# Kernel tuning notes

Measured on AMD Instinct MI355X. Metric: run time of the kernel, lower is better.

Reference implementation:

```python
import jax, jax.numpy as jnp
import numpy as np

B, S, D, H, HS = 4, 2048, 1024, 16, 64
DFF = 4 * D
EPS = 1e-5


def setup_inputs() -> dict:
    key = jax.random.key(0)
    ks = jax.random.split(key, 16)
    std = 0.02
    return {
        "x": jax.random.normal(ks[0], (B, S, D), jnp.float32),
        "Wq": jax.random.normal(ks[1], (H, D, HS), jnp.float32) * std,
        "bq": jnp.zeros((H, HS), jnp.float32),
        "Wk": jax.random.normal(ks[2], (H, D, HS), jnp.float32) * std,
        "bk": jnp.zeros((H, HS), jnp.float32),
        "Wv": jax.random.normal(ks[3], (H, D, HS), jnp.float32) * std,
        "bv": jnp.zeros((H, HS), jnp.float32),
        "Wp": jax.random.normal(ks[4], (D, D), jnp.float32) * std,
        "bp": jnp.zeros((D,), jnp.float32),
        "ln1_w": jnp.ones((D,), jnp.float32),
        "ln1_b": jnp.zeros((D,), jnp.float32),
        "ln2_w": jnp.ones((D,), jnp.float32),
        "ln2_b": jnp.zeros((D,), jnp.float32),
        "W1": jax.random.normal(ks[5], (D, DFF), jnp.float32) * std,
        "b1": jnp.zeros((DFF,), jnp.float32),
        "W2": jax.random.normal(ks[6], (DFF, D), jnp.float32) * std,
        "b2": jnp.zeros((D,), jnp.float32),
    }


def _layernorm(x, w, b):
    mu = jnp.mean(x, axis=-1, keepdims=True)
    var = jnp.mean(jnp.square(x - mu), axis=-1, keepdims=True)
    return (x - mu) * jax.lax.rsqrt(var + EPS) * w + b


def _block(x, Wq, bq, Wk, bk, Wv, bv, Wp, bp, ln1_w, ln1_b, ln2_w, ln2_b, W1, b1, W2, b2):
    seq = x.shape[1]
    xn = _layernorm(x, ln1_w, ln1_b)
    # batched per-head projections: [B,H,S,HS]
    q = jnp.einsum('bsd,hdk->bhsk', xn, Wq) + bq[:, None, :]
    k = jnp.einsum('bsd,hdk->bhsk', xn, Wk) + bk[:, None, :]
    v = jnp.einsum('bsd,hdk->bhsk', xn, Wv) + bv[:, None, :]
    scores = jnp.einsum('bhsk,bhtk->bhst', q, k)
    mask = jnp.tril(jnp.ones((seq, seq), bool))
    # original: masked_fill(-inf) then divide by sqrt(head_size) -> equivalent
    scores = jnp.where(mask, scores / jnp.sqrt(jnp.float32(HS)), -jnp.inf)
    attn = jax.nn.softmax(scores, axis=-1)
    out = jnp.einsum('bhst,bhtk->bhsk', attn, v)
    out = out.transpose(0, 2, 1, 3).reshape(x.shape[0], seq, H * HS)
    att = out @ Wp + bp
    x = x + att
    xn2 = _layernorm(x, ln2_w, ln2_b)
    h = jax.nn.gelu(xn2 @ W1 + b1, approximate=False)  # torch nn.GELU default = exact
    ffn = h @ W2 + b2
    return x + ffn


def reference(x, Wq, bq, Wk, bk, Wv, bv, Wp, bp, ln1_w, ln1_b, ln2_w, ln2_b, W1, b1, W2, b2):
    out = _block(x, Wq, bq, Wk, bk, Wv, bv, Wp, bp, ln1_w, ln1_b, ln2_w, ln2_b, W1, b1, W2, b2)
    return out
```

## Files before the change

### kernel.cpp

```cpp
#include <hip/hip_runtime.h>
#include <hip/hip_bf16.h>

#define D_MODEL 1024
#define SEQ 2048
#define NH 16
#define HSZ 64
#define DFF_ 4096

typedef __attribute__((ext_vector_type(8))) short short8;
typedef __attribute__((ext_vector_type(4))) short short4v;
typedef __attribute__((ext_vector_type(4))) float f32x4;

static __device__ __forceinline__ short f2bf(float f) {
  unsigned u = __builtin_bit_cast(unsigned, f);
  u = u + 0x7fffu + ((u >> 16) & 1u);
  return (short)(u >> 16);
}

static __device__ __forceinline__ unsigned packbf2(float a, float b) {
  return (unsigned)(unsigned short)f2bf(a) | ((unsigned)(unsigned short)f2bf(b) << 16);
}

static __device__ __forceinline__ f32x4 mfma16(short8 a, short8 b, f32x4 c) {
  return __builtin_amdgcn_mfma_f32_16x16x32_bf16(a, b, c, 0, 0, 0);
}

static __device__ __forceinline__ void gld16(const short* g, short* l) {
  __builtin_amdgcn_global_load_lds((const __attribute__((address_space(1))) void*)g,
                                   (__attribute__((address_space(3))) void*)l, 16, 0, 0);
}

#define SM_SCALE 0.18033688011112042f
#define VMW(n) asm volatile("s_waitcnt vmcnt(" #n ")" ::: "memory")

__global__ void transpose_qkv_kernel(const float* __restrict__ Wq, const float* __restrict__ Wk,
                                     const float* __restrict__ Wv, short* __restrict__ dst) {
  __shared__ float tile[32][33];
  const int z = blockIdx.z;
  const int which = z >> 4, hh = z & 15;
  const float* src = (which == 0 ? Wq : which == 1 ? Wk : Wv) + (long)hh * (D_MODEL * HSZ);
  const int c0 = blockIdx.x * 32, r0 = blockIdx.y * 32;
  const int tx = threadIdx.x, ty = threadIdx.y;
#pragma unroll
  for (int i = 0; i < 4; ++i)
    tile[ty + 8 * i][tx] = src[(long)(r0 + ty + 8 * i) * HSZ + c0 + tx];
  __syncthreads();
#pragma unroll
  for (int i = 0; i < 4; ++i)
    dst[((long)which * 1024 + hh * 64 + c0 + ty + 8 * i) * D_MODEL + r0 + tx] =
        f2bf(tile[tx][ty + 8 * i]);
}

__global__ void transpose_all_kernel(const float* __restrict__ Wp, short* __restrict__ WpT,
                                     const float* __restrict__ W1, short* __restrict__ W1T,
                                     const float* __restrict__ W2, short* __restrict__ W2T) {
  __shared__ float tile[32][33];
  int id = blockIdx.x;
  const float* src;
  short* dst;
  int R, C, bx, by;
  if (id < 1024) {
    src = Wp; dst = WpT; R = 1024; C = 1024; bx = id & 31; by = id >> 5;
  } else if (id < 5120) {
    id -= 1024;
    src = W1; dst = W1T; R = 1024; C = 4096; bx = id & 127; by = id >> 7;
  } else {
    id -= 5120;
    src = W2; dst = W2T; R = 4096; C = 1024; bx = id & 31; by = id >> 5;
  }
  const int c0 = bx * 32, r0 = by * 32;
  const int tx = threadIdx.x, ty = threadIdx.y;
#pragma unroll
  for (int i = 0; i < 4; ++i)
    tile[ty + 8 * i][tx] = src[(long)(r0 + ty + 8 * i) * C + c0 + tx];
  __syncthreads();
#pragma unroll
  for (int i = 0; i < 4; ++i)
    dst[(long)(c0 + ty + 8 * i) * R + r0 + tx] = f2bf(tile[tx][ty + 8 * i]);
}

__global__ void v_transpose_kernel(const short* __restrict__ vb, short* __restrict__ vt) {
  __shared__ short tile[64 * 72];
  const int bh = blockIdx.y;
  const int t0 = blockIdx.x * 64;
  const long base = (long)bh * SEQ * HSZ;
  const int tid = threadIdx.x;
  const int r = tid >> 3, c = (tid & 7) * 8;
#pragma unroll
  for (int it = 0; it < 2; ++it) {
    const int rr = r + it * 32;
    *(short8*)&tile[rr * 72 + c] = *(const short8*)(vb + base + (long)(t0 + rr) * HSZ + c);
  }
  __syncthreads();
#pragma unroll
  for (int it = 0; it < 2; ++it) {
    const int rr = r + it * 32;
    short8 o;
#pragma unroll
    for (int u = 0; u < 8; ++u) o[u] = tile[(c + u) * 72 + rr];
    *(short8*)(vt + base + (long)rr * SEQ + t0 + c) = o;
  }
}

__global__ void ln_kernel(const float* __restrict__ x, const float* __restrict__ w,
                          const float* __restrict__ b, short* __restrict__ out) {
  const int row = blockIdx.x;
  const float* xr = x + (size_t)row * D_MODEL;
  const int t = threadIdx.x;
  float4 v = *(const float4*)(xr + t * 4);
  float s = v.x + v.y + v.z + v.w;
  float s2 = v.x * v.x + v.y * v.y + v.z * v.z + v.w * v.w;
#pragma unroll
  for (int o = 1; o < 64; o <<= 1) {
    s += __shfl_xor(s, o, 64);
    s2 += __shfl_xor(s2, o, 64);
  }
  __shared__ float ps[8];
  const int lane = t & 63, wid = t >> 6;
  if (lane == 0) { ps[wid] = s; ps[wid + 4] = s2; }
  __syncthreads();
  s = ps[0] + ps[1] + ps[2] + ps[3];
  s2 = ps[4] + ps[5] + ps[6] + ps[7];
  const float mu = s * (1.0f / D_MODEL);
  const float var = s2 * (1.0f / D_MODEL) - mu * mu;
  const float rs = rsqrtf(var + 1e-5f);
  float4 wv = *(const float4*)(w + t * 4);
  float4 bv = *(const float4*)(b + t * 4);
  short4v o4;
  o4[0] = f2bf((v.x - mu) * rs * wv.x + bv.x);
  o4[1] = f2bf((v.y - mu) * rs * wv.y + bv.y);
  o4[2] = f2bf((v.z - mu) * rs * wv.z + bv.z);
  o4[3] = f2bf((v.w - mu) * rs * wv.w + bv.w);
  *(short4v*)(out + (size_t)row * D_MODEL + t * 4) = o4;
}

template <int MODE, int BM>
__global__ __launch_bounds__(512, 2) void gemm_kernel(
    const short* __restrict__ A, const short* __restrict__ Bt, const int K,
    const float* __restrict__ c0, const float* __restrict__ c1,
    const float* __restrict__ c2, const float* __restrict__ res,
    void* __restrict__ o0, void* __restrict__ o1, void* __restrict__ o2) {
  constexpr int NPH = BM / 64;
  constexpr int NA = BM / 64;
  constexpr int NTOT = NA + 4;
  constexpr int PER = NTOT / NPH;
  constexpr int HM = BM / 2;
  __shared__ short As[2][BM * 64];
  __shared__ short Bs[2][256 * 64];
  const long r0 = (long)blockIdx.y * BM;
  const long n0 = (long)blockIdx.x * 256;
  const int tid = threadIdx.x;
  const int lane = tid & 63, wid = tid >> 6;
  const int wm = wid >> 2, wn = wid & 3;
  const int l16 = lane & 15, lg = lane >> 4;

  long offA[NA], offB[4];
#pragma unroll
  for (int i = 0; i < NA; ++i) {
    const int c = tid + i * 512;
    const int lam = c >> 3, s = c & 7;
    const int cch = lam >> 6, rho = lam & 63;
    const int g = cch * 32 + (rho & 31) + ((rho >> 5) ? HM : 0);
    offA[i] = (long)(r0 + g) * K + ((s ^ (lam & 7)) << 3);
  }
#pragma unroll
  for (int i = 0; i < 4; ++i) {
    const int c = tid + i * 512;
    const int row = c >> 3, s = c & 7;
    offB[i] = (long)(n0 + row) * K + ((s ^ (row & 7)) << 3);
  }

  f32x4 acc[2 * NPH][4];
#pragma unroll
  for (int m = 0; m < 2 * NPH; ++m)
#pragma unroll
    for (int n = 0; n < 4; ++n) {
      f32x4 z = {0.f, 0.f, 0.f, 0.f};
      acc[m][n] = z;
    }

  const int x7 = l16 & 7;
  const int sw0 = (lg ^ x7) * 8, sw1 = ((4 + lg) ^ x7) * 8;

#define STG(j, kt, buf)                                                      \
  {                                                                          \
    if ((j) < 4)                                                             \
      gld16(Bt + offB[(j)] + (kt), &Bs[buf][(tid + (j)*512) * 8]);           \
    else                                                                     \
      gld16(A + offA[(j)-4] + (kt), &As[buf][(tid + ((j)-4) * 512) * 8]);    \
  }

#define GPHASE(P, ENDSTMT)                                                   \
  {                                                                          \
    short8 af[2][2];                                                         \
    _Pragma("unroll") for (int mm = 0; mm < 2; ++mm) {                       \
      const int lam = (P)*64 + wm * 32 + mm * 16 + l16;                      \
      af[mm][0] = *(const short8*)&Ap[lam * 64 + sw0];                       \
      af[mm][1] = *(const short8*)&Ap[lam * 64 + sw1];                       \
    }                                                                        \
    if ((P) == 0) {                                                          \
      _Pragma("unroll") for (int n = 0; n < 4; ++n) {                        \
        const int r = (wn * 64 + n * 16 + l16) * 64;                         \
        bf[n][0] = *(const short8*)&Bp[r + sw0];                             \
        bf[n][1] = *(const short8*)&Bp[r + sw1];                             \
      }                                                                      \
    }                                                                        \
    if (st) {                                                                \
      _Pragma("unroll") for (int j = (P)*PER; j < ((P) + 1) * PER; ++j)      \
          STG(j, ktn, nb);                                                   \
    }                                                                        \
    asm volatile("s_waitcnt lgkmcnt(0)" ::: "memory");                       \
    __builtin_amdgcn_sched_barrier(0);                                       \
    __builtin_amdgcn_s_setprio(1);                                           \
    _Pragma("unroll") for (int kk = 0; kk < 2; ++kk)                         \
        _Pragma("unroll") for (int mm = 0; mm < 2; ++mm)                     \
        _Pragma("unroll") for (int n = 0; n < 4; ++n) acc[2 * (P) + mm][n] = \
        mfma16(af[mm][kk], bf[n][kk], acc[2 * (P) + mm][n]);                 \
    __builtin_amdgcn_s_setprio(0);                                           \
    ENDSTMT;                                                                 \
    __builtin_amdgcn_s_barrier();                                            \
  }

  const int NT = K >> 6;
#pragma unroll
  for (int j = 0; j < NTOT; ++j) STG(j, 0, 0);
  if constexpr (BM == 256) VMW(3); else VMW(1);
  __builtin_amdgcn_s_barrier();

  for (int t = 0; t < NT; ++t) {
    const int cur = t & 1, nb = cur ^ 1;
    const short* Ap = As[cur];
    const short* Bp = Bs[cur];
    const bool st = (t + 1 < NT);
    const int ktn = (t + 1) << 6;
    short8 bf[4][2];
    if constexpr (BM == 256) {
      GPHASE(0, { if (st) VMW(4); else VMW(2); });
      GPHASE(1, { if (st) VMW(5); else VMW(1); });
      GPHASE(2, { if (st) VMW(6); else VMW(0); });
      GPHASE(3, { if (st) VMW(3); });
    } else {
      GPHASE(0, { if (st) VMW(3); else VMW(0); });
      GPHASE(1, { if (st) VMW(1); });
    }
  }
#undef GPHASE
#undef STG

#pragma unroll
  for (int m = 0; m < 2 * NPH; ++m) {
    const long rowb = r0 + wm * HM + m * 16 + lg * 4;
#pragma unroll
    for (int n = 0; n < 4; ++n) {
      const long col = n0 + wn * 64 + n * 16 + l16;
#pragma unroll
      for (int j = 0; j < 4; ++j) {
        float val = acc[m][n][j];
        const long rr = rowb + j;
        if (MODE == 0) {
          const int c10 = (int)col & 1023;
          const int which = (int)col >> 10;
          const float* bb = which == 0 ? c0 : which == 1 ? c1 : c2;
          short* oo = (short*)(which == 0 ? o0 : which == 1 ? o1 : o2);
          val += bb[c10];
          if (which == 0) val *= SM_SCALE;
          const long bidx = rr >> 11, sidx = rr & 2047;
          const int h = c10 >> 6, hs = c10 & 63;
          oo[(((bidx * NH) + h) * SEQ + sidx) * HSZ + hs] = f2bf(val);
        } else if (MODE == 1) {
          val += c0[col] + res[rr * D_MODEL + col];
          ((float*)o0)[rr * D_MODEL + col] = val;
        } else if (MODE == 2) {
          val += c0[col];
          const float g = 0.5f * val * (1.0f + erff(val * 0.70710678118654752f));
          ((short*)o0)[rr * DFF_ + col] = f2bf(g);
        } else {
          val += c0[col] + res[rr * D_MODEL + col];
          ((float*)o0)[rr * D_MODEL + col] = val;
        }
      }
    }
  }
}

__global__ void attn_kernel(const short* __restrict__ q, const short* __restrict__ k,
                            const short* __restrict__ vt, short* __restrict__ att) {
  const int qt = (SEQ / 128 - 1) - (int)blockIdx.y;
  const int bh = blockIdx.x;
  const int b = bh >> 4, h = bh & 15;
  const int tid = threadIdx.x;
  const int lane = tid & 63, wq = tid >> 6;
  const int l16 = lane & 15, lg = lane >> 4;
  const long base = (long)bh * SEQ * HSZ;

  __shared__ short Ks[64 * 64];
  __shared__ short Vts[64 * 64];
  __shared__ short Ps[4 * 32 * 72];
  short* Psw = &Ps[wq * 32 * 72];

  const int R0 = qt * 128 + wq * 32;

  short8 qf[2][2];
#pragma unroll
  for (int qn = 0; qn < 2; ++qn)
#pragma unroll
    for (int kk = 0; kk < 2; ++kk)
      qf[qn][kk] =
          *(const short8*)(q + base + (long)(R0 + qn * 16 + l16) * HSZ + kk * 32 + lg * 8);

  float m_[2] = {-INFINITY, -INFINITY};
  float l_[2] = {0.f, 0.f};
  f32x4 oacc[2][4];
#pragma unroll
  for (int qn = 0; qn < 2; ++qn)
#pragma unroll
    for (int hf = 0; hf < 4; ++hf) {
      f32x4 z = {0.f, 0.f, 0.f, 0.f};
      oacc[qn][hf] = z;
    }

  const int srow = tid >> 3, wg = tid & 7;
  const int swc = (wg ^ (srow & 7)) * 8;
  const int x7 = l16 & 7;
  const int rc0 = (lg ^ x7) * 8, rc1 = ((4 + lg) ^ x7) * 8;
  const int tend = (qt + 1) * 128;

  for (int t0 = 0; t0 < tend; t0 += 64) {
    __syncthreads();
#pragma unroll
    for (int it = 0; it < 2; ++it) {
      const int r = srow + it * 32;
      const short8 kv = *(const short8*)(k + base + (long)(t0 + r) * HSZ + wg * 8);
      const short8 vv = *(const short8*)(vt + base + (long)r * SEQ + t0 + wg * 8);
      *(short8*)&Ks[r * 64 + swc] = kv;
      *(short8*)&Vts[r * 64 + swc] = vv;
    }
    __syncthreads();

    if (t0 <= R0 + 31) {
      f32x4 sf[4][2];
#pragma unroll
      for (int tt = 0; tt < 4; ++tt)
#pragma unroll
        for (int qn = 0; qn < 2; ++qn) {
          f32x4 z = {0.f, 0.f, 0.f, 0.f};
          sf[tt][qn] = z;
        }
      __builtin_amdgcn_s_setprio(1);
#pragma unroll
      for (int kk = 0; kk < 2; ++kk)
#pragma unroll
        for (int tt = 0; tt < 4; ++tt) {
          short8 kf = *(const short8*)&Ks[(tt * 16 + l16) * 64 + (kk ? rc1 : rc0)];
#pragma unroll
          for (int qn = 0; qn < 2; ++qn) sf[tt][qn] = mfma16(kf, qf[qn][kk], sf[tt][qn]);
        }
      __builtin_amdgcn_s_setprio(0);

      const bool domask = (t0 + 63 > R0);
      if (domask) {
        const int tb = t0 + lg * 4;
#pragma unroll
        for (int tt = 0; tt < 4; ++tt)
#pragma unroll
          for (int qn = 0; qn < 2; ++qn) {
            const int qg = R0 + qn * 16 + l16;
#pragma unroll
            for (int j = 0; j < 4; ++j)
              if (tb + tt * 16 + j > qg) sf[tt][qn][j] = -INFINITY;
          }
      }

      float mx[2];
#pragma unroll
      for (int qn = 0; qn < 2; ++qn) {
        float m0 = sf[0][qn][0];
#pragma unroll
        for (int tt = 0; tt < 4; ++tt)
#pragma unroll
          for (int j = 0; j < 4; ++j) m0 = fmaxf(m0, sf[tt][qn][j]);
        m0 = fmaxf(m0, __shfl_xor(m0, 16, 64));
        m0 = fmaxf(m0, __shfl_xor(m0, 32, 64));
        mx[qn] = m0;
      }
      const int ok = (mx[0] <= m_[0] + 8.f) && (mx[1] <= m_[1] + 8.f);
      if (!__all(ok)) {
#pragma unroll
        for (int qn = 0; qn < 2; ++qn) {
          const float mnew = fmaxf(m_[qn], mx[qn]);
          const float rc = exp2f(m_[qn] - mnew);
          m_[qn] = mnew;
          l_[qn] *= rc;
#pragma unroll
          for (int hf = 0; hf < 4; ++hf)
#pragma unroll
            for (int j = 0; j < 4; ++j) oacc[qn][hf][j] *= rc;
        }
      }
#pragma unroll
      for (int qn = 0; qn < 2; ++qn) {
        float sum = 0.f;
#pragma unroll
        for (int tt = 0; tt < 4; ++tt)
#pragma unroll
          for (int j = 0; j < 4; ++j) {
            const float p = exp2f(sf[tt][qn][j] - m_[qn]);
            sf[tt][qn][j] = p;
            sum += p;
          }
        l_[qn] += sum;
      }

#pragma unroll
      for (int qn = 0; qn < 2; ++qn)
#pragma unroll
        for (int tt = 0; tt < 4; ++tt) {
          const int ro = (qn * 16 + l16) * 72 + tt * 16 + lg * 4;
          *(unsigned*)&Psw[ro] = packbf2(sf[tt][qn][0], sf[tt][qn][1]);
          *(unsigned*)&Psw[ro + 2] = packbf2(sf[tt][qn][2], sf[tt][qn][3]);
        }

      __builtin_amdgcn_s_setprio(1);
#pragma unroll
      for (int kk = 0; kk < 2; ++kk) {
        short8 pa[2];
#pragma unroll
        for (int qn = 0; qn < 2; ++qn)
          pa[qn] = *(const short8*)&Psw[(qn * 16 + l16) * 72 + kk * 32 + lg * 8];
#pragma unroll
        for (int hf = 0; hf < 4; ++hf) {
          short8 vf = *(const short8*)&Vts[(hf * 16 + l16) * 64 + (kk ? rc1 : rc0)];
#pragma unroll
          for (int qn = 0; qn < 2; ++qn)
            oacc[qn][hf] = mfma16(vf, pa[qn], oacc[qn][hf]);
        }
      }
      __builtin_amdgcn_s_setprio(0);
    }
  }

#pragma unroll
  for (int qn = 0; qn < 2; ++qn) {
    float lt = l_[qn];
    lt += __shfl_xor(lt, 16, 64);
    lt += __shfl_xor(lt, 32, 64);
    const float inv = 1.0f / lt;
    const long row = R0 + qn * 16 + l16;
#pragma unroll
    for (int hf = 0; hf < 4; ++hf) {
      short4v o4;
#pragma unroll
      for (int j = 0; j < 4; ++j) o4[j] = f2bf(oacc[qn][hf][j] * inv);
      *(short4v*)(att + ((long)b * SEQ + row) * D_MODEL + h * HSZ + hf * 16 + lg * 4) = o4;
    }
  }
}

extern "C" void kernel_launch(void* const* d_in, const int* in_sizes, int n_in,
                              void* d_out, int out_size, void* d_ws, size_t ws_size,
                              hipStream_t stream) {
  const float* x = (const float*)d_in[0];
  const float* Wq = (const float*)d_in[1];
  const float* bq = (const float*)d_in[2];
  const float* Wk = (const float*)d_in[3];
  const float* bk = (const float*)d_in[4];
  const float* Wv = (const float*)d_in[5];
  const float* bv = (const float*)d_in[6];
  const float* Wp = (const float*)d_in[7];
  const float* bp = (const float*)d_in[8];
  const float* g1 = (const float*)d_in[9];
  const float* be1 = (const float*)d_in[10];
  const float* g2 = (const float*)d_in[11];
  const float* be2 = (const float*)d_in[12];
  const float* W1 = (const float*)d_in[13];
  const float* b1 = (const float*)d_in[14];
  const float* W2 = (const float*)d_in[15];
  const float* b2 = (const float*)d_in[16];
  float* out = (float*)d_out;
  char* ws = (char*)d_ws;

  if (ws_size < 209715200ull) return;

  short* WqkvT = (short*)(ws + 0);
  short* WpT = (short*)(ws + 6291456);
  short* W1T = (short*)(ws + 8388608);
  short* W2T = (short*)(ws + 16777216);
  short* xn = (short*)(ws + 25165824);
  short* vt = (short*)(ws + 25165824);
  short* qb = (short*)(ws + 41943040);
  short* kb = (short*)(ws + 58720256);
  short* vb = (short*)(ws + 75497472);
  short* att = (short*)(ws + 92274688);
  float* x1 = (float*)(ws + 109051904);
  short* hb = (short*)(ws + 142606336);

  dim3 tb(32, 8);
  transpose_qkv_kernel<<<dim3(2, 32, 48), tb, 0, stream>>>(Wq, Wk, Wv, WqkvT);
  transpose_all_kernel<<<9216, tb, 0, stream>>>(Wp, WpT, W1, W1T, W2, W2T);
  ln_kernel<<<8192, 256, 0, stream>>>(x, g1, be1, xn);
  gemm_kernel<0, 128><<<dim3(12, 64), 512, 0, stream>>>(xn, WqkvT, 1024, bq, bk, bv,
                                                        nullptr, qb, kb, vb);
  v_transpose_kernel<<<dim3(32, 64), 256, 0, stream>>>(vb, vt);
  attn_kernel<<<dim3(64, 16), 256, 0, stream>>>(qb, kb, vt, att);
  gemm_kernel<1, 128><<<dim3(4, 64), 512, 0, stream>>>(att, WpT, 1024, bp, nullptr,
                                                       nullptr, x, x1, nullptr, nullptr);
  ln_kernel<<<8192, 256, 0, stream>>>(x1, g2, be2, xn);
  gemm_kernel<2, 256><<<dim3(16, 32), 512, 0, stream>>>(xn, W1T, 1024, b1, nullptr,
                                                        nullptr, nullptr, hb, nullptr,
                                                        nullptr);
  gemm_kernel<3, 128><<<dim3(4, 64), 512, 0, stream>>>(hb, W2T, 4096, b2, nullptr,
                                                       nullptr, x1, out, nullptr, nullptr);
}
```

Before: 407.7 us.

## Add 128x128-tile GEMM kernel for the projection and FFN-down GEMMs

Adds a dedicated GEMM kernel with 128x128 output tiles, double-buffered LDS staging of 64-wide K slices, and XOR-swizzled shared memory. It replaces the old generic gemm_kernel (128x256 N-tiles, 256 blocks) for the attention output projection and the FFN second GEMM, and the launch grid doubles to 512 blocks. The aim is better CU occupancy and more parallelism for these N=1024 GEMMs. The cost is more redundant A-tile loads per output, and each block does less work.

```diff
diff --git a/kernel.cpp b/kernel.cpp
--- a/kernel.cpp
+++ b/kernel.cpp
@@ -267,9 +267,6 @@
           const long bidx = rr >> 11, sidx = rr & 2047;
           const int h = c10 >> 6, hs = c10 & 63;
           oo[(((bidx * NH) + h) * SEQ + sidx) * HSZ + hs] = f2bf(val);
-        } else if (MODE == 1) {
-          val += c0[col] + res[rr * D_MODEL + col];
-          ((float*)o0)[rr * D_MODEL + col] = val;
         } else if (MODE == 2) {
           val += c0[col];
           const float g = 0.5f * val * (1.0f + erff(val * 0.70710678118654752f));
@@ -278,6 +275,103 @@
           val += c0[col] + res[rr * D_MODEL + col];
           ((float*)o0)[rr * D_MODEL + col] = val;
         }
+      }
+    }
+  }
+}
+
+__global__ __launch_bounds__(512, 2) void gemm128_kernel(
+    const short* __restrict__ A, const short* __restrict__ Bt, const int K,
+    const float* __restrict__ c0, const float* __restrict__ res,
+    float* __restrict__ o0) {
+  __shared__ short As[2][128 * 64];
+  __shared__ short Bs[2][128 * 64];
+  const long r0 = (long)blockIdx.y * 128;
+  const long n0 = (long)blockIdx.x * 128;
+  const int tid = threadIdx.x;
+  const int lane = tid & 63, wid = tid >> 6;
+  const int wm = wid >> 1, wn = wid & 1;
+  const int l16 = lane & 15, lg = lane >> 4;
+
+  long offA[2], offB[2];
+#pragma unroll
+  for (int i = 0; i < 2; ++i) {
+    const int c = tid + i * 512;
+    const int lam = c >> 3, s = c & 7;
+    offA[i] = (long)(r0 + lam) * K + ((s ^ (lam & 7)) << 3);
+    offB[i] = (long)(n0 + lam) * K + ((s ^ (lam & 7)) << 3);
+  }
+
+  f32x4 acc[2][4];
+#pragma unroll
+  for (int m = 0; m < 2; ++m)
+#pragma unroll
+    for (int n = 0; n < 4; ++n) {
+      f32x4 z = {0.f, 0.f, 0.f, 0.f};
+      acc[m][n] = z;
+    }
+
+  const int x7 = l16 & 7;
+  const int sw0 = (lg ^ x7) * 8, sw1 = ((4 + lg) ^ x7) * 8;
+
+#define STG8(kt, buf)                                                       \
+  {                                                                         \
+    _Pragma("unroll") for (int i = 0; i < 2; ++i) {                         \
+      gld16(Bt + offB[i] + (kt), &Bs[buf][(tid + i * 512) * 8]);            \
+      gld16(A + offA[i] + (kt), &As[buf][(tid + i * 512) * 8]);             \
+    }                                                                       \
+  }
+
+  const int NT = K >> 6;
+  STG8(0, 0);
+  VMW(0);
+  __builtin_amdgcn_s_barrier();
+
+  for (int t = 0; t < NT; ++t) {
+    const int cur = t & 1, nb = cur ^ 1;
+    const short* Ap = As[cur];
+    const short* Bp = Bs[cur];
+    const bool st = (t + 1 < NT);
+    if (st) STG8((t + 1) << 6, nb);
+    short8 af[2][2], bf[4][2];
+#pragma unroll
+    for (int mm = 0; mm < 2; ++mm) {
+      const int r = (wm * 32 + mm * 16 + l16) * 64;
+      af[mm][0] = *(const short8*)&Ap[r + sw0];
+      af[mm][1] = *(const short8*)&Ap[r + sw1];
+    }
+#pragma unroll
+    for (int n = 0; n < 4; ++n) {
+      const int r = (wn * 64 + n * 16 + l16) * 64;
+      bf[n][0] = *(const short8*)&Bp[r + sw0];
+      bf[n][1] = *(const short8*)&Bp[r + sw1];
+    }
+    asm volatile("s_waitcnt lgkmcnt(0)" ::: "memory");
+    __builtin_amdgcn_sched_barrier(0);
+    __builtin_amdgcn_s_setprio(1);
+#pragma unroll
+    for (int kk = 0; kk < 2; ++kk)
+#pragma unroll
+      for (int mm = 0; mm < 2; ++mm)
+#pragma unroll
+        for (int n = 0; n < 4; ++n)
+          acc[mm][n] = mfma16(af[mm][kk], bf[n][kk], acc[mm][n]);
+    __builtin_amdgcn_s_setprio(0);
+    if (st) VMW(0);
+    __builtin_amdgcn_s_barrier();
+  }
+#undef STG8
+
+#pragma unroll
+  for (int mm = 0; mm < 2; ++mm) {
+    const long rowb = r0 + wm * 32 + mm * 16 + lg * 4;
+#pragma unroll
+    for (int n = 0; n < 4; ++n) {
+      const long col = n0 + wn * 64 + n * 16 + l16;
+#pragma unroll
+      for (int j = 0; j < 4; ++j) {
+        const long rr = rowb + j;
+        o0[rr * D_MODEL + col] = acc[mm][n][j] + c0[col] + res[rr * D_MODEL + col];
       }
     }
   }
@@ -502,12 +596,10 @@
                                                         nullptr, qb, kb, vb);
   v_transpose_kernel<<<dim3(32, 64), 256, 0, stream>>>(vb, vt);
   attn_kernel<<<dim3(64, 16), 256, 0, stream>>>(qb, kb, vt, att);
-  gemm_kernel<1, 128><<<dim3(4, 64), 512, 0, stream>>>(att, WpT, 1024, bp, nullptr,
-                                                       nullptr, x, x1, nullptr, nullptr);
+  gemm128_kernel<<<dim3(8, 64), 512, 0, stream>>>(att, WpT, 1024, bp, x, x1);
   ln_kernel<<<8192, 256, 0, stream>>>(x1, g2, be2, xn);
   gemm_kernel<2, 256><<<dim3(16, 32), 512, 0, stream>>>(xn, W1T, 1024, b1, nullptr,
                                                         nullptr, nullptr, hb, nullptr,
                                                         nullptr);
-  gemm_kernel<3, 128><<<dim3(4, 64), 512, 0, stream>>>(hb, W2T, 4096, b2, nullptr,
-                                                       nullptr, x1, out, nullptr, nullptr);
-}
+  gemm128_kernel<<<dim3(8, 64), 512, 0, stream>>>(hb, W2T, 4096, b2, x1, out);
+}
```

Result: no change. 405.7 us, median of 4 (-0.5%).
